# Performance work log

Measured on AMD Instinct MI355X. Metric: run time of the kernel, lower is better.

Reference implementation:

```python
import jax, jax.numpy as jnp
import numpy as np

B, S, D, E, TOP_K = 4, 2048, 768, 8, 2
H = 4 * D  # expert hidden dim


def setup_inputs() -> dict:
    key = jax.random.key(0)
    ks = jax.random.split(key, 12)
    s = 0.02
    return {
        "x": jax.random.normal(ks[0], (B, S, D), dtype=jnp.float32),
        "noise": jax.random.normal(ks[1], (B, S, E), dtype=jnp.float32),
        "w_route": jax.random.normal(ks[2], (D, E), dtype=jnp.float32) * s,
        "b_route": jnp.zeros((E,), dtype=jnp.float32),
        "w_noise": jax.random.normal(ks[3], (D, E), dtype=jnp.float32) * s,
        "b_noise": jnp.zeros((E,), dtype=jnp.float32),
        "W1": jax.random.normal(ks[4], (E, D, H), dtype=jnp.float32) * s,
        "b1": jnp.zeros((E, H), dtype=jnp.float32),
        "W2": jax.random.normal(ks[5], (E, H, D), dtype=jnp.float32) * s,
        "b2": jnp.zeros((E, D), dtype=jnp.float32),
    }


def reference(x, noise, w_route, b_route, w_noise, b_noise, W1, b1, W2, b2):
    # Noisy top-k router
    logits = x @ w_route + b_route                      # [B,S,E]
    noise_scale = jax.nn.softplus(x @ w_noise + b_noise)
    noisy = logits + noise * noise_scale
    top_v, top_i = jax.lax.top_k(noisy, TOP_K)          # [B,S,k]
    sel = jax.nn.one_hot(top_i, E, dtype=jnp.bool_).any(axis=-2)  # [B,S,E]
    sparse_logits = jnp.where(sel, noisy, -jnp.inf)
    gates = jax.nn.softmax(sparse_logits, axis=-1)      # zeros off top-k

    # Combine expert outputs weighted by gates (gate=0 for unselected experts,
    # so math matches the masked gather/scatter loop in the original).
    out = jnp.zeros_like(x)
    for e in range(E):  # fixed small expert count
        h = jax.nn.relu(x @ W1[e] + b1[e])              # [B,S,H]
        y = h @ W2[e] + b2[e]                           # [B,S,D]
        out = out + gates[..., e:e + 1] * y
    return out
```

## Files before the change

### kernel.cpp

```cpp
#include <hip/hip_runtime.h>
#include <hip/hip_bf16.h>
#include <stdint.h>

#define DD 768
#define EE 8
#define HHID 3072
#define NTOK 8192
#define CAP 16384
#define HROWS 3072

typedef __attribute__((ext_vector_type(8))) short bshort8;
typedef __attribute__((ext_vector_type(4))) float f32x4;

typedef __attribute__((address_space(1))) const unsigned int g_u32;
typedef __attribute__((address_space(3))) unsigned int l_u32;

__device__ __forceinline__ void glds16(const void* g, void* l) {
    __builtin_amdgcn_global_load_lds((g_u32*)g, (l_u32*)l, 16, 0, 0);
}

__device__ __forceinline__ unsigned short f2bf(float f) {
    unsigned int u = __float_as_uint(f);
    u += 0x7fffu + ((u >> 16) & 1u);
    return (unsigned short)(u >> 16);
}

__global__ __launch_bounds__(256) void router_score(
    const float* __restrict__ x, const float* __restrict__ noise,
    const float* __restrict__ w_route, const float* __restrict__ b_route,
    const float* __restrict__ w_noise, const float* __restrict__ b_noise,
    int2* __restrict__ eidx, float2* __restrict__ gates,
    unsigned short* __restrict__ xbf)
{
    const int lane = threadIdx.x & 63;
    const int wv = threadIdx.x >> 6;
    const int t = blockIdx.x * 4 + wv;

    float aR[EE], aN[EE];
#pragma unroll
    for (int e = 0; e < EE; ++e) { aR[e] = 0.f; aN[e] = 0.f; }

    const float* xr = x + (size_t)t * DD;
    unsigned short* xb = xbf + (size_t)t * DD;
#pragma unroll 4
    for (int d = lane; d < DD; d += 64) {
        float xv = xr[d];
        xb[d] = f2bf(xv);
        const float4* wr = reinterpret_cast<const float4*>(w_route + d * EE);
        const float4* wn = reinterpret_cast<const float4*>(w_noise + d * EE);
        float4 r0 = wr[0], r1 = wr[1];
        float4 n0 = wn[0], n1 = wn[1];
        aR[0] += xv * r0.x; aR[1] += xv * r0.y; aR[2] += xv * r0.z; aR[3] += xv * r0.w;
        aR[4] += xv * r1.x; aR[5] += xv * r1.y; aR[6] += xv * r1.z; aR[7] += xv * r1.w;
        aN[0] += xv * n0.x; aN[1] += xv * n0.y; aN[2] += xv * n0.z; aN[3] += xv * n0.w;
        aN[4] += xv * n1.x; aN[5] += xv * n1.y; aN[6] += xv * n1.z; aN[7] += xv * n1.w;
    }
#pragma unroll
    for (int e = 0; e < EE; ++e) {
#pragma unroll
        for (int off = 32; off > 0; off >>= 1) {
            aR[e] += __shfl_xor(aR[e], off);
            aN[e] += __shfl_xor(aN[e], off);
        }
    }

    if (lane == 0) {
        float nv[EE];
#pragma unroll
        for (int e = 0; e < EE; ++e) {
            float z = aN[e] + b_noise[e];
            float sp = (z > 20.f) ? z : log1pf(expf(z));
            nv[e] = aR[e] + b_route[e] + noise[(size_t)t * EE + e] * sp;
        }
        int e1 = 0; float v1 = nv[0];
#pragma unroll
        for (int e = 1; e < EE; ++e) if (nv[e] > v1) { v1 = nv[e]; e1 = e; }
        int e2 = -1; float v2 = 0.f;
#pragma unroll
        for (int e = 0; e < EE; ++e) {
            if (e == e1) continue;
            if (e2 < 0 || nv[e] > v2) { v2 = nv[e]; e2 = e; }
        }
        float ex = expf(v2 - v1);
        float inv = 1.f / (1.f + ex);
        int2 ee; ee.x = e1; ee.y = e2;
        float2 gg; gg.x = inv; gg.y = ex * inv;
        eidx[t] = ee;
        gates[t] = gg;
    }
}

__global__ __launch_bounds__(1024) void scatter_kernel(
    const int2* __restrict__ eidx, const float2* __restrict__ gates,
    int* __restrict__ cnt, int* __restrict__ tlist, float* __restrict__ glist)
{
    __shared__ int lcnt[EE];
    const int tid = threadIdx.x;
    if (tid < EE) lcnt[tid] = 0;
    __syncthreads();
    const int lane = tid & 63;
    const int wv = tid >> 6;
    const unsigned long long lowmask = (1ull << lane) - 1ull;

    for (int it = 0; it < NTOK / 1024; ++it) {
        int t = it * 1024 + wv * 64 + lane;
        int2 ee = eidx[t];
        float2 gg = gates[t];
#pragma unroll
        for (int e = 0; e < EE; ++e) {
            unsigned long long m1 = __ballot(ee.x == e);
            unsigned long long m2 = __ballot(ee.y == e);
            int c1 = __popcll(m1);
            int c2 = __popcll(m2);
            int base = 0;
            if (lane == 0 && (c1 + c2) > 0) base = atomicAdd(&lcnt[e], c1 + c2);
            base = __shfl(base, 0);
            if (ee.x == e) {
                int pos = base + __popcll(m1 & lowmask);
                tlist[e * CAP + pos] = t; glist[e * CAP + pos] = gg.x;
            }
            if (ee.y == e) {
                int pos = base + c1 + __popcll(m2 & lowmask);
                tlist[e * CAP + pos] = t; glist[e * CAP + pos] = gg.y;
            }
        }
    }
    __syncthreads();
    if (tid < EE) cnt[tid] = lcnt[tid];
}

__global__ __launch_bounds__(256) void wconv_kernel(
    const float* __restrict__ W1, const float* __restrict__ W2,
    unsigned short* __restrict__ W1T, unsigned short* __restrict__ W2T)
{
    __shared__ unsigned short t2[64][80];
    const int bid = blockIdx.x;
    const int mat = bid / 1152;
    const int r0 = bid % 1152;
    const float* src; unsigned short* dst; int R, C, tr, tc;
    if (r0 < 576) {
        src = W1 + (size_t)mat * DD * HHID; dst = W1T + (size_t)mat * DD * HHID;
        R = DD; C = HHID; tr = r0 / 48; tc = r0 % 48;
    } else {
        int r1 = r0 - 576;
        src = W2 + (size_t)mat * DD * HHID; dst = W2T + (size_t)mat * DD * HHID;
        R = HHID; C = DD; tr = r1 / 12; tc = r1 % 12;
    }
    const int tid = threadIdx.x;
    {
        const int r = tid >> 2;
        const int c0 = (tid & 3) * 16;
        const float* srow = src + (size_t)(tr * 64 + r) * C + tc * 64 + c0;
#pragma unroll
        for (int j = 0; j < 16; j += 4) {
            float4 v = *reinterpret_cast<const float4*>(srow + j);
            t2[c0 + j + 0][r] = f2bf(v.x);
            t2[c0 + j + 1][r] = f2bf(v.y);
            t2[c0 + j + 2][r] = f2bf(v.z);
            t2[c0 + j + 3][r] = f2bf(v.w);
        }
    }
    __syncthreads();
    {
        const int c = tid >> 2;
        const int ch = (tid & 3) * 16;
        unsigned short* drow = dst + (size_t)(tc * 64 + c) * R + tr * 64 + ch;
#pragma unroll
        for (int j = 0; j < 16; j += 8)
            *reinterpret_cast<uint4*>(drow + j) = *reinterpret_cast<const uint4*>(&t2[c][ch + j]);
    }
}

__global__ __launch_bounds__(512, 4) void gemm1_kernel(
    const unsigned short* __restrict__ xbf,
    const unsigned short* __restrict__ W1T,
    const float* __restrict__ b1,
    const int* __restrict__ cnt, const int* __restrict__ tlist,
    unsigned short* __restrict__ hbuf,
    int hp0, int hpass)
{
    __shared__ __align__(16) unsigned short As[2][128 * 64];
    __shared__ __align__(16) unsigned short Bs[2][128 * 64];

    const int e = blockIdx.x & 7;
    const int tile = blockIdx.x >> 3;
    const int mt = tile % 24;
    const int nt = tile / 24;
    int n = cnt[e]; n = n < HROWS ? n : HROWS;
    const int mbase = mt * 128;
    if (mbase >= n) return;
    const int nbase = nt * 128;

    const int tid = threadIdx.x;
    const int lane = tid & 63;
    const int w = tid >> 6;
    const int r_lo = lane >> 3;
    const int ch = lane & 7;

    const char* pa[2]; const char* pb[2];
#pragma unroll
    for (int i = 0; i < 2; ++i) {
        int r = w * 16 + i * 8 + r_lo;
        int slot = mbase + r;
        int cs = slot < n ? slot : n - 1;
        int tok = tlist[e * CAP + cs];
        pa[i] = (const char*)xbf + (size_t)tok * 1536 + ((ch ^ (r & 7)) << 4);
        int hcol = hp0 + nbase + r;
        pb[i] = (const char*)W1T + ((size_t)(e * HHID + hcol)) * 1536 + ((ch ^ (r & 7)) << 4);
    }

    const int wm = w & 1;
    const int wn = w >> 1;
    const int r15 = lane & 15;
    const int kq = lane >> 4;

    f32x4 acc[4][2];
#pragma unroll
    for (int mf = 0; mf < 4; ++mf)
#pragma unroll
        for (int nf = 0; nf < 2; ++nf)
            acc[mf][nf] = (f32x4)0.f;

    auto STAGE = [&](int buf) {
        unsigned short* al = &As[buf][w * 16 * 64];
        unsigned short* bl = &Bs[buf][w * 16 * 64];
        glds16(pa[0], al);            glds16(pa[1], al + 512);
        glds16(pb[0], bl);            glds16(pb[1], bl + 512);
        pa[0] += 128; pa[1] += 128; pb[0] += 128; pb[1] += 128;
    };
    auto COMPUTE = [&](int buf) {
        const char* Ab = (const char*)As[buf];
        const char* Bb = (const char*)Bs[buf];
#pragma unroll
        for (int s = 0; s < 2; ++s) {
            bshort8 af[4], bfr[2];
#pragma unroll
            for (int mf = 0; mf < 4; ++mf) {
                int row = wm * 64 + mf * 16 + r15;
                af[mf] = *(const bshort8*)(Ab + row * 128 + (((s * 4 + kq) ^ (row & 7)) << 4));
            }
#pragma unroll
            for (int nf = 0; nf < 2; ++nf) {
                int row = wn * 32 + nf * 16 + r15;
                bfr[nf] = *(const bshort8*)(Bb + row * 128 + (((s * 4 + kq) ^ (row & 7)) << 4));
            }
#pragma unroll
            for (int mf = 0; mf < 4; ++mf)
#pragma unroll
                for (int nf = 0; nf < 2; ++nf)
                    acc[mf][nf] = __builtin_amdgcn_mfma_f32_16x16x32_bf16(af[mf], bfr[nf], acc[mf][nf], 0, 0, 0);
        }
    };

    STAGE(0);
    int cur = 0;
#pragma unroll 1
    for (int t = 0; t < 11; ++t) {
        STAGE(cur ^ 1);
        asm volatile("s_waitcnt vmcnt(4)" ::: "memory");
        __builtin_amdgcn_s_barrier();
        asm volatile("" ::: "memory");
        COMPUTE(cur);
        asm volatile("" ::: "memory");
        __builtin_amdgcn_s_barrier();
        asm volatile("" ::: "memory");
        cur ^= 1;
    }
    asm volatile("s_waitcnt vmcnt(0)" ::: "memory");
    __builtin_amdgcn_s_barrier();
    asm volatile("" ::: "memory");
    COMPUTE(cur);

#pragma unroll
    for (int nf = 0; nf < 2; ++nf) {
        int col = nbase + wn * 32 + nf * 16 + r15;
        float bb = b1[e * HHID + hp0 + col];
#pragma unroll
        for (int mf = 0; mf < 4; ++mf) {
            int rowb = mbase + wm * 64 + mf * 16 + kq * 4;
#pragma unroll
            for (int rr = 0; rr < 4; ++rr) {
                float v = fmaxf(acc[mf][nf][rr] + bb, 0.f);
                hbuf[((size_t)(e * HROWS + rowb + rr)) * hpass + col] = f2bf(v);
            }
        }
    }
}

__global__ __launch_bounds__(512, 4) void gemm2_kernel(
    const unsigned short* __restrict__ hbuf,
    const unsigned short* __restrict__ W2T,
    const float* __restrict__ b2,
    const int* __restrict__ cnt, const int* __restrict__ tlist,
    const float* __restrict__ glist, float* __restrict__ out,
    int hp0, int hpass, int addb2)
{
    __shared__ __align__(16) unsigned short As[2][128 * 64];
    __shared__ __align__(16) unsigned short Bs[2][128 * 64];

    const int e = blockIdx.x & 7;
    const int tile = blockIdx.x >> 3;
    const int mt = tile % 24;
    const int nt = tile / 24;
    int n = cnt[e]; n = n < HROWS ? n : HROWS;
    const int mbase = mt * 128;
    if (mbase >= n) return;
    const int nbase = nt * 128;

    const int tid = threadIdx.x;
    const int lane = tid & 63;
    const int w = tid >> 6;
    const int r_lo = lane >> 3;
    const int ch = lane & 7;
    const size_t hrow_b = (size_t)hpass * 2;

    const char* pa[2]; const char* pb[2];
#pragma unroll
    for (int i = 0; i < 2; ++i) {
        int r = w * 16 + i * 8 + r_lo;
        pa[i] = (const char*)hbuf + (size_t)(e * HROWS + mbase + r) * hrow_b + ((ch ^ (r & 7)) << 4);
        int d = nbase + r;
        pb[i] = (const char*)W2T + ((size_t)(e * DD + d)) * 6144 + (size_t)hp0 * 2 + ((ch ^ (r & 7)) << 4);
    }

    const int wm = w & 1;
    const int wn = w >> 1;
    const int r15 = lane & 15;
    const int kq = lane >> 4;

    f32x4 acc[4][2];
#pragma unroll
    for (int mf = 0; mf < 4; ++mf)
#pragma unroll
        for (int nf = 0; nf < 2; ++nf)
            acc[mf][nf] = (f32x4)0.f;

    auto STAGE = [&](int buf) {
        unsigned short* al = &As[buf][w * 16 * 64];
        unsigned short* bl = &Bs[buf][w * 16 * 64];
        glds16(pa[0], al);            glds16(pa[1], al + 512);
        glds16(pb[0], bl);            glds16(pb[1], bl + 512);
        pa[0] += 128; pa[1] += 128; pb[0] += 128; pb[1] += 128;
    };
    auto COMPUTE = [&](int buf) {
        const char* Ab = (const char*)As[buf];
        const char* Bb = (const char*)Bs[buf];
#pragma unroll
        for (int s = 0; s < 2; ++s) {
            bshort8 af[4], bfr[2];
#pragma unroll
            for (int mf = 0; mf < 4; ++mf) {
                int row = wm * 64 + mf * 16 + r15;
                af[mf] = *(const bshort8*)(Ab + row * 128 + (((s * 4 + kq) ^ (row & 7)) << 4));
            }
#pragma unroll
            for (int nf = 0; nf < 2; ++nf) {
                int row = wn * 32 + nf * 16 + r15;
                bfr[nf] = *(const bshort8*)(Bb + row * 128 + (((s * 4 + kq) ^ (row & 7)) << 4));
            }
#pragma unroll
            for (int mf = 0; mf < 4; ++mf)
#pragma unroll
                for (int nf = 0; nf < 2; ++nf)
                    acc[mf][nf] = __builtin_amdgcn_mfma_f32_16x16x32_bf16(af[mf], bfr[nf], acc[mf][nf], 0, 0, 0);
        }
    };

    const int NK = hpass >> 6;
    STAGE(0);
    int cur = 0;
#pragma unroll 1
    for (int t = 0; t < NK - 1; ++t) {
        STAGE(cur ^ 1);
        asm volatile("s_waitcnt vmcnt(4)" ::: "memory");
        __builtin_amdgcn_s_barrier();
        asm volatile("" ::: "memory");
        COMPUTE(cur);
        asm volatile("" ::: "memory");
        __builtin_amdgcn_s_barrier();
        asm volatile("" ::: "memory");
        cur ^= 1;
    }
    asm volatile("s_waitcnt vmcnt(0)" ::: "memory");
    __builtin_amdgcn_s_barrier();
    asm volatile("" ::: "memory");
    COMPUTE(cur);

    float bb[2];
#pragma unroll
    for (int nf = 0; nf < 2; ++nf) {
        int d = nbase + wn * 32 + nf * 16 + r15;
        bb[nf] = addb2 ? b2[e * DD + d] : 0.f;
    }
#pragma unroll
    for (int mf = 0; mf < 4; ++mf) {
#pragma unroll
        for (int rr = 0; rr < 4; ++rr) {
            int slot = mbase + wm * 64 + mf * 16 + kq * 4 + rr;
            if (slot < n) {
                int tok = tlist[e * CAP + slot];
                float g = glist[e * CAP + slot];
                float* orow = out + (size_t)tok * DD;
#pragma unroll
                for (int nf = 0; nf < 2; ++nf) {
                    int d = nbase + wn * 32 + nf * 16 + r15;
                    atomicAdd(orow + d, g * (acc[mf][nf][rr] + bb[nf]));
                }
            }
        }
    }
}

extern "C" void kernel_launch(void* const* d_in, const int* in_sizes, int n_in,
                              void* d_out, int out_size, void* d_ws, size_t ws_size,
                              hipStream_t stream) {
    const float* x       = (const float*)d_in[0];
    const float* noise   = (const float*)d_in[1];
    const float* w_route = (const float*)d_in[2];
    const float* b_route = (const float*)d_in[3];
    const float* w_noise = (const float*)d_in[4];
    const float* b_noise = (const float*)d_in[5];
    const float* W1      = (const float*)d_in[6];
    const float* b1      = (const float*)d_in[7];
    const float* W2      = (const float*)d_in[8];
    const float* b2      = (const float*)d_in[9];
    float* out = (float*)d_out;

    char* ws = (char*)d_ws;
    int*    cnt   = (int*)ws;
    int*    tlist = (int*)(ws + 1024);
    float*  glist = (float*)(ws + 1024 + (size_t)CAP * EE * 4);
    int2*   eidx  = (int2*)(ws + 1024 + (size_t)CAP * EE * 8);
    float2* gates = (float2*)(ws + 1024 + (size_t)CAP * EE * 8 + (size_t)NTOK * 8);

    const size_t OFF_W1T = (size_t)2 << 20;
    const size_t SZ_W    = (size_t)EE * DD * HHID * 2;
    const size_t OFF_W2T = OFF_W1T + SZ_W;
    const size_t OFF_XBF = OFF_W2T + SZ_W;
    const size_t SZ_XBF  = (size_t)NTOK * DD * 2;
    const size_t OFF_HB  = OFF_XBF + SZ_XBF;
    unsigned short* W1T = (unsigned short*)(ws + OFF_W1T);
    unsigned short* W2T = (unsigned short*)(ws + OFF_W2T);
    unsigned short* xbf = (unsigned short*)(ws + OFF_XBF);
    unsigned short* hbuf = (unsigned short*)(ws + OFF_HB);

    const size_t HB_FULL = (size_t)EE * HROWS * HHID * 2;
    size_t hav = (ws_size > OFF_HB) ? ws_size - OFF_HB : 0;
    int npass = 0;
    if      (hav >= HB_FULL)      npass = 1;
    else if (hav >= HB_FULL / 2)  npass = 2;
    else if (hav >= HB_FULL / 4)  npass = 4;
    else if (hav >= HB_FULL / 8)  npass = 8;
    else                          npass = 12;

    hipMemsetAsync(d_out, 0, (size_t)out_size * sizeof(float), stream);

    router_score<<<NTOK / 4, 256, 0, stream>>>(x, noise, w_route, b_route,
                                               w_noise, b_noise, eidx, gates, xbf);
    scatter_kernel<<<1, 1024, 0, stream>>>(eidx, gates, cnt, tlist, glist);
    wconv_kernel<<<EE * 1152, 256, 0, stream>>>(W1, W2, W1T, W2T);

    const int hpass = HHID / npass;
    for (int p = 0; p < npass; ++p) {
        gemm1_kernel<<<24 * (hpass / 128) * 8, 512, 0, stream>>>(
            xbf, W1T, b1, cnt, tlist, hbuf, p * hpass, hpass);
        gemm2_kernel<<<24 * 6 * 8, 512, 0, stream>>>(
            hbuf, W2T, b2, cnt, tlist, glist, out, p * hpass, hpass, p == 0 ? 1 : 0);
    }
}
```

Measured before the change: 522.3 us.

## Use 256x128 tiles with triple-buffered LDS pipeline in expert GEMMs

Both expert GEMM kernels now compute 256x128 output tiles instead of 128x128, doubling the M fragments per wave. The global-to-LDS prefetch becomes a three-stage ring with loads split across two compute phases, and MFMA sections are wrapped in s_setprio. The aim is more operand reuse per LDS load and better hiding of global latency. In exchange, LDS use per block rises and occupancy drops to 2 blocks per CU, the grid halves in size, and partial-tile waste grows when an expert has few tokens.

```diff
diff --git a/kernel.cpp b/kernel.cpp
--- a/kernel.cpp
+++ b/kernel.cpp
@@ -171,7 +171,55 @@
     }
 }
 
-__global__ __launch_bounds__(512, 4) void gemm1_kernel(
+#define SA_(buf, i) { glds16(pa[i], &As[buf][(i) * 4096 + w * 512]); pa[i] += 128; }
+#define SB_(buf, j) { glds16(pb[j], &Bs[buf][(j) * 4096 + w * 512]); pb[j] += 128; }
+#define PH_(buf, P) { \
+    const char* Ab = (const char*)As[buf]; \
+    const char* Bb = (const char*)Bs[buf]; \
+    _Pragma("unroll") \
+    for (int s = 0; s < 2; ++s) { \
+        bshort8 af[4], bfr[2]; \
+        _Pragma("unroll") \
+        for (int mfl = 0; mfl < 4; ++mfl) { \
+            int row = wm * 128 + ((P) * 4 + mfl) * 16 + r15; \
+            af[mfl] = *(const bshort8*)(Ab + row * 128 + (((s * 4 + kq) ^ (row & 7)) << 4)); \
+        } \
+        _Pragma("unroll") \
+        for (int nf = 0; nf < 2; ++nf) { \
+            int row = wn * 32 + nf * 16 + r15; \
+            bfr[nf] = *(const bshort8*)(Bb + row * 128 + (((s * 4 + kq) ^ (row & 7)) << 4)); \
+        } \
+        __builtin_amdgcn_s_setprio(1); \
+        _Pragma("unroll") \
+        for (int mfl = 0; mfl < 4; ++mfl) \
+            _Pragma("unroll") \
+            for (int nf = 0; nf < 2; ++nf) \
+                acc[(P) * 4 + mfl][nf] = __builtin_amdgcn_mfma_f32_16x16x32_bf16(af[mfl], bfr[nf], acc[(P) * 4 + mfl][nf], 0, 0, 0); \
+        __builtin_amdgcn_s_setprio(0); \
+    } }
+
+#define GEMM_LOOP(NKv) \
+    SA_(0, 0) SA_(0, 1) SA_(0, 2) SA_(0, 3) SB_(0, 0) SB_(0, 1) \
+    SA_(1, 0) SA_(1, 1) SA_(1, 2) SA_(1, 3) SB_(1, 0) SB_(1, 1) \
+    asm volatile("s_waitcnt vmcnt(6)" ::: "memory"); \
+    __builtin_amdgcn_s_barrier(); \
+    { int bc = 0, bs = 2; \
+    _Pragma("unroll 1") \
+    for (int kt = 0; kt < (NKv); ++kt) { \
+        int st = (kt + 2) < (NKv); \
+        if (st) { SA_(bs, 0) SA_(bs, 1) SA_(bs, 2) } \
+        PH_(bc, 0); \
+        __builtin_amdgcn_s_barrier(); \
+        if (st) { SA_(bs, 3) SB_(bs, 0) SB_(bs, 1) } \
+        PH_(bc, 1); \
+        if (kt + 2 < (NKv))      { asm volatile("s_waitcnt vmcnt(6)" ::: "memory"); } \
+        else if (kt + 1 < (NKv)) { asm volatile("s_waitcnt vmcnt(0)" ::: "memory"); } \
+        __builtin_amdgcn_s_barrier(); \
+        bc = bc == 2 ? 0 : bc + 1; \
+        bs = bs == 2 ? 0 : bs + 1; \
+    } }
+
+__global__ __launch_bounds__(512, 2) void gemm1_kernel(
     const unsigned short* __restrict__ xbf,
     const unsigned short* __restrict__ W1T,
     const float* __restrict__ b1,
@@ -179,34 +227,38 @@
     unsigned short* __restrict__ hbuf,
     int hp0, int hpass)
 {
-    __shared__ __align__(16) unsigned short As[2][128 * 64];
-    __shared__ __align__(16) unsigned short Bs[2][128 * 64];
+    __shared__ __align__(16) unsigned short As[3][256 * 64];
+    __shared__ __align__(16) unsigned short Bs[3][128 * 64];
 
     const int e = blockIdx.x & 7;
     const int tile = blockIdx.x >> 3;
-    const int mt = tile % 24;
-    const int nt = tile / 24;
+    const int mt = tile % 12;
+    const int nt = tile / 12;
     int n = cnt[e]; n = n < HROWS ? n : HROWS;
-    const int mbase = mt * 128;
+    const int mbase = mt * 256;
     if (mbase >= n) return;
     const int nbase = nt * 128;
 
     const int tid = threadIdx.x;
     const int lane = tid & 63;
     const int w = tid >> 6;
-    const int r_lo = lane >> 3;
-    const int ch = lane & 7;
-
-    const char* pa[2]; const char* pb[2];
-#pragma unroll
-    for (int i = 0; i < 2; ++i) {
-        int r = w * 16 + i * 8 + r_lo;
+    const int rl = tid >> 3;
+    const int ch = tid & 7;
+
+    const char* pa[4]; const char* pb[2];
+#pragma unroll
+    for (int i = 0; i < 4; ++i) {
+        int r = i * 64 + rl;
         int slot = mbase + r;
         int cs = slot < n ? slot : n - 1;
         int tok = tlist[e * CAP + cs];
         pa[i] = (const char*)xbf + (size_t)tok * 1536 + ((ch ^ (r & 7)) << 4);
+    }
+#pragma unroll
+    for (int j = 0; j < 2; ++j) {
+        int r = j * 64 + rl;
         int hcol = hp0 + nbase + r;
-        pb[i] = (const char*)W1T + ((size_t)(e * HHID + hcol)) * 1536 + ((ch ^ (r & 7)) << 4);
+        pb[j] = (const char*)W1T + ((size_t)(e * HHID + hcol)) * 1536 + ((ch ^ (r & 7)) << 4);
     }
 
     const int wm = w & 1;
@@ -214,70 +266,22 @@
     const int r15 = lane & 15;
     const int kq = lane >> 4;
 
-    f32x4 acc[4][2];
-#pragma unroll
-    for (int mf = 0; mf < 4; ++mf)
+    f32x4 acc[8][2];
+#pragma unroll
+    for (int mf = 0; mf < 8; ++mf)
 #pragma unroll
         for (int nf = 0; nf < 2; ++nf)
             acc[mf][nf] = (f32x4)0.f;
 
-    auto STAGE = [&](int buf) {
-        unsigned short* al = &As[buf][w * 16 * 64];
-        unsigned short* bl = &Bs[buf][w * 16 * 64];
-        glds16(pa[0], al);            glds16(pa[1], al + 512);
-        glds16(pb[0], bl);            glds16(pb[1], bl + 512);
-        pa[0] += 128; pa[1] += 128; pb[0] += 128; pb[1] += 128;
-    };
-    auto COMPUTE = [&](int buf) {
-        const char* Ab = (const char*)As[buf];
-        const char* Bb = (const char*)Bs[buf];
-#pragma unroll
-        for (int s = 0; s < 2; ++s) {
-            bshort8 af[4], bfr[2];
-#pragma unroll
-            for (int mf = 0; mf < 4; ++mf) {
-                int row = wm * 64 + mf * 16 + r15;
-                af[mf] = *(const bshort8*)(Ab + row * 128 + (((s * 4 + kq) ^ (row & 7)) << 4));
-            }
-#pragma unroll
-            for (int nf = 0; nf < 2; ++nf) {
-                int row = wn * 32 + nf * 16 + r15;
-                bfr[nf] = *(const bshort8*)(Bb + row * 128 + (((s * 4 + kq) ^ (row & 7)) << 4));
-            }
-#pragma unroll
-            for (int mf = 0; mf < 4; ++mf)
-#pragma unroll
-                for (int nf = 0; nf < 2; ++nf)
-                    acc[mf][nf] = __builtin_amdgcn_mfma_f32_16x16x32_bf16(af[mf], bfr[nf], acc[mf][nf], 0, 0, 0);
-        }
-    };
-
-    STAGE(0);
-    int cur = 0;
-#pragma unroll 1
-    for (int t = 0; t < 11; ++t) {
-        STAGE(cur ^ 1);
-        asm volatile("s_waitcnt vmcnt(4)" ::: "memory");
-        __builtin_amdgcn_s_barrier();
-        asm volatile("" ::: "memory");
-        COMPUTE(cur);
-        asm volatile("" ::: "memory");
-        __builtin_amdgcn_s_barrier();
-        asm volatile("" ::: "memory");
-        cur ^= 1;
-    }
-    asm volatile("s_waitcnt vmcnt(0)" ::: "memory");
-    __builtin_amdgcn_s_barrier();
-    asm volatile("" ::: "memory");
-    COMPUTE(cur);
+    GEMM_LOOP(12)
 
 #pragma unroll
     for (int nf = 0; nf < 2; ++nf) {
         int col = nbase + wn * 32 + nf * 16 + r15;
         float bb = b1[e * HHID + hp0 + col];
 #pragma unroll
-        for (int mf = 0; mf < 4; ++mf) {
-            int rowb = mbase + wm * 64 + mf * 16 + kq * 4;
+        for (int mf = 0; mf < 8; ++mf) {
+            int rowb = mbase + wm * 128 + mf * 16 + kq * 4;
 #pragma unroll
             for (int rr = 0; rr < 4; ++rr) {
                 float v = fmaxf(acc[mf][nf][rr] + bb, 0.f);
@@ -287,7 +291,7 @@
     }
 }
 
-__global__ __launch_bounds__(512, 4) void gemm2_kernel(
+__global__ __launch_bounds__(512, 2) void gemm2_kernel(
     const unsigned short* __restrict__ hbuf,
     const unsigned short* __restrict__ W2T,
     const float* __restrict__ b2,
@@ -295,32 +299,36 @@
     const float* __restrict__ glist, float* __restrict__ out,
     int hp0, int hpass, int addb2)
 {
-    __shared__ __align__(16) unsigned short As[2][128 * 64];
-    __shared__ __align__(16) unsigned short Bs[2][128 * 64];
+    __shared__ __align__(16) unsigned short As[3][256 * 64];
+    __shared__ __align__(16) unsigned short Bs[3][128 * 64];
 
     const int e = blockIdx.x & 7;
     const int tile = blockIdx.x >> 3;
-    const int mt = tile % 24;
-    const int nt = tile / 24;
+    const int mt = tile % 12;
+    const int nt = tile / 12;
     int n = cnt[e]; n = n < HROWS ? n : HROWS;
-    const int mbase = mt * 128;
+    const int mbase = mt * 256;
     if (mbase >= n) return;
     const int nbase = nt * 128;
 
     const int tid = threadIdx.x;
     const int lane = tid & 63;
     const int w = tid >> 6;
-    const int r_lo = lane >> 3;
-    const int ch = lane & 7;
+    const int rl = tid >> 3;
+    const int ch = tid & 7;
     const size_t hrow_b = (size_t)hpass * 2;
 
-    const char* pa[2]; const char* pb[2];
-#pragma unroll
-    for (int i = 0; i < 2; ++i) {
-        int r = w * 16 + i * 8 + r_lo;
+    const char* pa[4]; const char* pb[2];
+#pragma unroll
+    for (int i = 0; i < 4; ++i) {
+        int r = i * 64 + rl;
         pa[i] = (const char*)hbuf + (size_t)(e * HROWS + mbase + r) * hrow_b + ((ch ^ (r & 7)) << 4);
+    }
+#pragma unroll
+    for (int j = 0; j < 2; ++j) {
+        int r = j * 64 + rl;
         int d = nbase + r;
-        pb[i] = (const char*)W2T + ((size_t)(e * DD + d)) * 6144 + (size_t)hp0 * 2 + ((ch ^ (r & 7)) << 4);
+        pb[j] = (const char*)W2T + ((size_t)(e * DD + d)) * 6144 + (size_t)hp0 * 2 + ((ch ^ (r & 7)) << 4);
     }
 
     const int wm = w & 1;
@@ -328,63 +336,15 @@
     const int r15 = lane & 15;
     const int kq = lane >> 4;
 
-    f32x4 acc[4][2];
-#pragma unroll
-    for (int mf = 0; mf < 4; ++mf)
+    f32x4 acc[8][2];
+#pragma unroll
+    for (int mf = 0; mf < 8; ++mf)
 #pragma unroll
         for (int nf = 0; nf < 2; ++nf)
             acc[mf][nf] = (f32x4)0.f;
 
-    auto STAGE = [&](int buf) {
-        unsigned short* al = &As[buf][w * 16 * 64];
-        unsigned short* bl = &Bs[buf][w * 16 * 64];
-        glds16(pa[0], al);            glds16(pa[1], al + 512);
-        glds16(pb[0], bl);            glds16(pb[1], bl + 512);
-        pa[0] += 128; pa[1] += 128; pb[0] += 128; pb[1] += 128;
-    };
-    auto COMPUTE = [&](int buf) {
-        const char* Ab = (const char*)As[buf];
-        const char* Bb = (const char*)Bs[buf];
-#pragma unroll
-        for (int s = 0; s < 2; ++s) {
-            bshort8 af[4], bfr[2];
-#pragma unroll
-            for (int mf = 0; mf < 4; ++mf) {
-                int row = wm * 64 + mf * 16 + r15;
-                af[mf] = *(const bshort8*)(Ab + row * 128 + (((s * 4 + kq) ^ (row & 7)) << 4));
-            }
-#pragma unroll
-            for (int nf = 0; nf < 2; ++nf) {
-                int row = wn * 32 + nf * 16 + r15;
-                bfr[nf] = *(const bshort8*)(Bb + row * 128 + (((s * 4 + kq) ^ (row & 7)) << 4));
-            }
-#pragma unroll
-            for (int mf = 0; mf < 4; ++mf)
-#pragma unroll
-                for (int nf = 0; nf < 2; ++nf)
-                    acc[mf][nf] = __builtin_amdgcn_mfma_f32_16x16x32_bf16(af[mf], bfr[nf], acc[mf][nf], 0, 0, 0);
-        }
-    };
-
     const int NK = hpass >> 6;
-    STAGE(0);
-    int cur = 0;
-#pragma unroll 1
-    for (int t = 0; t < NK - 1; ++t) {
-        STAGE(cur ^ 1);
-        asm volatile("s_waitcnt vmcnt(4)" ::: "memory");
-        __builtin_amdgcn_s_barrier();
-        asm volatile("" ::: "memory");
-        COMPUTE(cur);
-        asm volatile("" ::: "memory");
-        __builtin_amdgcn_s_barrier();
-        asm volatile("" ::: "memory");
-        cur ^= 1;
-    }
-    asm volatile("s_waitcnt vmcnt(0)" ::: "memory");
-    __builtin_amdgcn_s_barrier();
-    asm volatile("" ::: "memory");
-    COMPUTE(cur);
+    GEMM_LOOP(NK)
 
     float bb[2];
 #pragma unroll
@@ -393,10 +353,10 @@
         bb[nf] = addb2 ? b2[e * DD + d] : 0.f;
     }
 #pragma unroll
-    for (int mf = 0; mf < 4; ++mf) {
+    for (int mf = 0; mf < 8; ++mf) {
 #pragma unroll
         for (int rr = 0; rr < 4; ++rr) {
-            int slot = mbase + wm * 64 + mf * 16 + kq * 4 + rr;
+            int slot = mbase + wm * 128 + mf * 16 + kq * 4 + rr;
             if (slot < n) {
                 int tok = tlist[e * CAP + slot];
                 float g = glist[e * CAP + slot];
@@ -462,9 +422,9 @@
 
     const int hpass = HHID / npass;
     for (int p = 0; p < npass; ++p) {
-        gemm1_kernel<<<24 * (hpass / 128) * 8, 512, 0, stream>>>(
+        gemm1_kernel<<<12 * (hpass / 128) * 8, 512, 0, stream>>>(
             xbf, W1T, b1, cnt, tlist, hbuf, p * hpass, hpass);
-        gemm2_kernel<<<24 * 6 * 8, 512, 0, stream>>>(
+        gemm2_kernel<<<12 * 6 * 8, 512, 0, stream>>>(
             hbuf, W2T, b2, cnt, tlist, glist, out, p * hpass, hpass, p == 0 ? 1 : 0);
     }
 }
```

Result: slower. 745.1 us (+42.7%).
